# Kernel tuning notes

Hardware: AMD Instinct MI355X
Metric: run time of the kernel (lower is better)

The kernel has to match this reference:

```python
import jax, jax.numpy as jnp
import numpy as np
from jax.scipy.special import logsumexp

D = 1024      # d_model
H = 8         # num_heads
N = 16        # state_dim
ITERS = 5     # sinkhorn_iters
TAU = 1.0
B, S = 4, 1024
EPS = 1e-5


def setup_inputs() -> dict:
    key = jax.random.key(0)
    ks = jax.random.split(key, 8)
    x = jax.random.normal(ks[0], (B, S, D), dtype=jnp.float32)
    ln_w = jnp.ones((D,), jnp.float32)
    ln_b = jnp.zeros((D,), jnp.float32)
    # perm_proj: normal std=0.01, zero bias
    Wp = 0.01 * jax.random.normal(ks[1], (D, H * N * N), dtype=jnp.float32)
    bp = jnp.zeros((H * N * N,), jnp.float32)
    # gate_proj: normal std=0.01, bias=2.0
    Wg = 0.01 * jax.random.normal(ks[2], (D, H * N), dtype=jnp.float32)
    bg = jnp.full((H * N,), 2.0, jnp.float32)
    # input_proj / output_proj: xavier uniform, zero bias
    lim_i = float(np.sqrt(6.0 / (D + H * N)))
    Wi = jax.random.uniform(ks[3], (D, H * N), jnp.float32, -lim_i, lim_i)
    bi = jnp.zeros((H * N,), jnp.float32)
    Wo = jax.random.uniform(ks[4], (H * N, D), jnp.float32, -lim_i, lim_i)
    bo = jnp.zeros((D,), jnp.float32)
    return {"x": x, "ln_w": ln_w, "ln_b": ln_b, "Wp": Wp, "bp": bp,
            "Wg": Wg, "bg": bg, "Wi": Wi, "bi": bi, "Wo": Wo, "bo": bo}


def _sinkhorn(log_alpha):
    # log-space Sinkhorn: alternate row/column normalization
    for _ in range(ITERS):
        log_alpha = log_alpha - logsumexp(log_alpha, axis=-1, keepdims=True)
        log_alpha = log_alpha - logsumexp(log_alpha, axis=-2, keepdims=True)
    return jnp.exp(log_alpha)


def reference(x, ln_w, ln_b, Wp, bp, Wg, bg, Wi, bi, Wo, bo):
    residual = x
    # LayerNorm
    mu = jnp.mean(x, axis=-1, keepdims=True)
    var = jnp.var(x, axis=-1, keepdims=True)
    xn = (x - mu) * jax.lax.rsqrt(var + EPS) * ln_w + ln_b
    # projections
    logits = ((xn @ Wp + bp).reshape(B, S, H, N, N)) / TAU
    gamma = jax.nn.sigmoid((xn @ Wg + bg).reshape(B, S, H, N))
    b_in = (xn @ Wi + bi).reshape(B, S, H, N)
    # Sinkhorn for all timesteps at once (independent of recurrent state)
    soft = _sinkhorn(logits)                      # [B,S,H,N,N]
    # sequential state update over time
    Ps = jnp.moveaxis(soft, 1, 0)                 # [S,B,H,N,N]
    gs = jnp.moveaxis(gamma, 1, 0)                # [S,B,H,N]
    bs = jnp.moveaxis(b_in, 1, 0)                 # [S,B,H,N]

    def step(h, inp):
        P, g, b = inp
        h_perm = jnp.einsum('bhij,bhj->bhi', P, h)
        h_new = g * h_perm + (1.0 - g) * b
        return h_new, h_new

    h0 = jnp.zeros((B, H, N), x.dtype)
    _, hs = jax.lax.scan(step, h0, (Ps, gs, bs))  # hs: [S,B,H,N]
    out = jnp.moveaxis(hs, 0, 1).reshape(B, S, H * N)
    out = out @ Wo + bo                           # dropout = identity (eval)
    return residual + out
```

## Files before the change

kernel.cpp:

```cpp
#include <hip/hip_runtime.h>
#include <hip/hip_bf16.h>

#define D_    1024
#define H_    8
#define N_    16
#define B_    4
#define S_    1024
#define TOK   (B_*S_)
#define NPROJ 2304
#define CHUNK 32
#define NCHUNK (S_/CHUNK)
#define NCHAIN (B_*H_)

typedef __attribute__((ext_vector_type(8))) short bf16x8;
typedef __attribute__((ext_vector_type(4))) float f32x4;

typedef __attribute__((address_space(3))) void       as3_void;
typedef const __attribute__((address_space(1))) void as1_void;

__device__ __forceinline__ void gload_lds16(const void* g, void* l) {
    __builtin_amdgcn_global_load_lds((as1_void*)g, (as3_void*)l, 16, 0, 0);
}

__device__ __forceinline__ short f2bf(float f) {
    unsigned u = __builtin_bit_cast(unsigned, f);
    unsigned r = 0x7FFFu + ((u >> 16) & 1u);
    return (short)((u + r) >> 16);
}
__device__ __forceinline__ float bf2f(short s) {
    unsigned u = ((unsigned)(unsigned short)s) << 16;
    return __builtin_bit_cast(float, u);
}

template <int IMM>
__device__ __forceinline__ float swzf(float x) {
    return __builtin_bit_cast(float,
        __builtin_amdgcn_ds_swizzle(__builtin_bit_cast(int, x), IMM));
}
__device__ __forceinline__ float bpermf(int addr, float x) {
    return __builtin_bit_cast(float,
        __builtin_amdgcn_ds_bpermute(addr, __builtin_bit_cast(int, x)));
}
template <int CTRL>
__device__ __forceinline__ float dppmov(float x) {
    return __builtin_bit_cast(float,
        __builtin_amdgcn_update_dpp(0, __builtin_bit_cast(int, x),
                                    CTRL, 0xF, 0xF, true));
}
#define DPP_QX1  0xB1
#define DPP_QX2  0x4E
#define DPP_HMIR 0x141
#define DPP_ROR8 0x128

__global__ __launch_bounds__(256) void tcast_all(const float* __restrict__ Wp,
                                                 const float* __restrict__ Wg,
                                                 const float* __restrict__ Wi,
                                                 const float* __restrict__ Wo,
                                                 short* __restrict__ WcatT,
                                                 short* __restrict__ WoT) {
    int id = blockIdx.x;
    const float* src; short* dst; int srcW, Ksz, n_off, bx, by;
    if (id < 2048)      { src = Wp; dst = WcatT; srcW = 2048; Ksz = 1024; n_off = 0;
                          bx = id & 63;  by = id >> 6; }
    else if (id < 2176) { int q = id - 2048; src = Wg; dst = WcatT; srcW = 128; Ksz = 1024;
                          n_off = 2048; bx = q & 3; by = q >> 2; }
    else if (id < 2304) { int q = id - 2176; src = Wi; dst = WcatT; srcW = 128; Ksz = 1024;
                          n_off = 2176; bx = q & 3; by = q >> 2; }
    else                { int q = id - 2304; src = Wo; dst = WoT; srcW = 1024; Ksz = 128;
                          n_off = 0; bx = q & 31; by = q >> 5; }
    __shared__ float tile[32][33];
    int n0 = bx * 32, k0 = by * 32;
    int r  = threadIdx.x >> 3;
    int c4 = (threadIdx.x & 7) * 4;
    float4 v = *(const float4*)(src + (size_t)(k0 + r) * srcW + n0 + c4);
    tile[r][c4+0] = v.x; tile[r][c4+1] = v.y; tile[r][c4+2] = v.z; tile[r][c4+3] = v.w;
    __syncthreads();
    short4 o;
    o.x = f2bf(tile[c4+0][r]); o.y = f2bf(tile[c4+1][r]);
    o.z = f2bf(tile[c4+2][r]); o.w = f2bf(tile[c4+3][r]);
    *(short4*)(dst + (size_t)(n_off + n0 + r) * Ksz + k0 + c4) = o;
}

__global__ __launch_bounds__(256) void ln_kernel(const float* __restrict__ x,
                                                 const float* __restrict__ w,
                                                 const float* __restrict__ b,
                                                 short* __restrict__ xn) {
    int row = blockIdx.x;
    int t = threadIdx.x;
    const float* xr = x + (size_t)row * D_;
    float4 v = *(const float4*)(xr + t * 4);
    float s  = v.x + v.y + v.z + v.w;
    float s2 = v.x*v.x + v.y*v.y + v.z*v.z + v.w*v.w;
    #pragma unroll
    for (int m = 1; m < 64; m <<= 1) { s += __shfl_xor(s, m); s2 += __shfl_xor(s2, m); }
    __shared__ float ps[4], ps2[4];
    if ((t & 63) == 0) { ps[t >> 6] = s; ps2[t >> 6] = s2; }
    __syncthreads();
    s  = ps[0] + ps[1] + ps[2] + ps[3];
    s2 = ps2[0] + ps2[1] + ps2[2] + ps2[3];
    float mu  = s * (1.0f / D_);
    float var = s2 * (1.0f / D_) - mu * mu;
    float inv = rsqrtf(var + 1e-5f);
    float4 wv = *(const float4*)(w + t * 4);
    float4 bv = *(const float4*)(b + t * 4);
    short4 o;
    o.x = f2bf((v.x - mu) * inv * wv.x + bv.x);
    o.y = f2bf((v.y - mu) * inv * wv.y + bv.y);
    o.z = f2bf((v.z - mu) * inv * wv.z + bv.z);
    o.w = f2bf((v.w - mu) * inv * wv.w + bv.w);
    *(short4*)(xn + (size_t)row * D_ + t * 4) = o;
}

template <int MODE>
__global__ __launch_bounds__(512) void gemm_bt(const short* __restrict__ A,
                                               const short* __restrict__ BT,
                                               void* __restrict__ Cout,
                                               int M, int N, int K,
                                               const float* __restrict__ bias0,
                                               const float* __restrict__ bias1,
                                               const float* __restrict__ bias2,
                                               const float* __restrict__ resid) {
    __shared__ short lA[2][128 * 32];
    __shared__ short lB[2][128 * 32];
    const int nwg = gridDim.x;
    const int cpx = nwg >> 3;
    const int orig = blockIdx.x;
    const int wg = (orig & 7) * cpx + (orig >> 3);
    const int ntn = N >> 7;
    const int m0 = (wg / ntn) * 128, n0 = (wg % ntn) * 128;
    const int t = threadIdx.x, w = t >> 6, l = t & 63;
    const int wm = w >> 2, wn = w & 3;
    const int sr = l >> 2;
    const int sg = (l & 3) ^ ((l >> 3) & 3);
    const int fr = l & 15, fg = l >> 4;
    const int frag_off = fr * 32 + 8 * (fg ^ ((fr >> 1) & 3));

    f32x4 acc[4][2];
    #pragma unroll
    for (int mi = 0; mi < 4; ++mi)
        #pragma unroll
        for (int ni = 0; ni < 2; ++ni) acc[mi][ni] = (f32x4){0.f, 0.f, 0.f, 0.f};

    auto STAGE = [&](int bi, int k0) {
        int row = w * 16 + sr;
        gload_lds16(A  + (size_t)(m0 + row) * K + k0 + sg * 8, &lA[bi][w * 512]);
        gload_lds16(BT + (size_t)(n0 + row) * K + k0 + sg * 8, &lB[bi][w * 512]);
    };

    const int NT = K >> 5;
    STAGE(0, 0);
    if (NT > 1) STAGE(1, 32);
    asm volatile("s_waitcnt vmcnt(2)" ::: "memory");
    __builtin_amdgcn_s_barrier();

    int cur = 0;
    for (int kt = 0; kt < NT; ++kt) {
        bf16x8 af[4], bfr[2];
        #pragma unroll
        for (int mi = 0; mi < 4; ++mi)
            af[mi] = *(const bf16x8*)(&lA[cur][(wm * 4 + mi) * 512] + frag_off);
        #pragma unroll
        for (int ni = 0; ni < 2; ++ni)
            bfr[ni] = *(const bf16x8*)(&lB[cur][(wn * 2 + ni) * 512] + frag_off);
        asm volatile("s_waitcnt lgkmcnt(0)" ::: "memory");
        __builtin_amdgcn_sched_barrier(0);
        __builtin_amdgcn_s_barrier();
        if (kt + 2 < NT) STAGE(cur, (kt + 2) << 5);
        __builtin_amdgcn_s_setprio(1);
        #pragma unroll
        for (int mi = 0; mi < 4; ++mi)
            #pragma unroll
            for (int ni = 0; ni < 2; ++ni)
                acc[mi][ni] = __builtin_amdgcn_mfma_f32_16x16x32_bf16(af[mi], bfr[ni], acc[mi][ni], 0, 0, 0);
        __builtin_amdgcn_s_setprio(0);
        if (kt + 1 < NT) {
            if (kt + 2 < NT) asm volatile("s_waitcnt vmcnt(2)" ::: "memory");
            else             asm volatile("s_waitcnt vmcnt(0)" ::: "memory");
            __builtin_amdgcn_sched_barrier(0);
            __builtin_amdgcn_s_barrier();
        }
        cur ^= 1;
    }

    const int cr = (l >> 4) * 4, cc = l & 15;
    #pragma unroll
    for (int mi = 0; mi < 4; ++mi)
        #pragma unroll
        for (int ni = 0; ni < 2; ++ni) {
            int col = n0 + wn * 32 + ni * 16 + cc;
            float badd;
            if (MODE == 0)
                badd = (col < 2048) ? bias0[col] : (col < 2176 ? bias1[col - 2048] : bias2[col - 2176]);
            else
                badd = bias0[col];
            #pragma unroll
            for (int e = 0; e < 4; ++e) {
                int row = m0 + wm * 64 + mi * 16 + cr + e;
                float vout = acc[mi][ni][e] + badd;
                if (MODE == 0) {
                    ((short*)Cout)[(size_t)row * N + col] = f2bf(vout);
                } else {
                    vout += resid[(size_t)row * N + col];
                    ((float*)Cout)[(size_t)row * N + col] = vout;
                }
            }
        }
}

__global__ __launch_bounds__(256) void sinkhorn_kernel(const short* __restrict__ Cp,
                                                       short* __restrict__ Ahat,
                                                       float* __restrict__ u) {
    int w = threadIdx.x >> 6, l = threadIdx.x & 63;
    int id = blockIdx.x * 4 + w;
    int r = id >> 3, hh = id & 7;
    int a = l >> 3, b = l & 7;
    const short* base = Cp + (size_t)r * NPROJ + hh * 256;
    short2 q0 = *(const short2*)(base + (2 * a)     * 16 + 2 * b);
    short2 q1 = *(const short2*)(base + (2 * a + 1) * 16 + 2 * b);
    float p00 = __expf(bf2f(q0.x)), p01 = __expf(bf2f(q0.y));
    float p10 = __expf(bf2f(q1.x)), p11 = __expf(bf2f(q1.y));
    const int a32 = ((l ^ 32) << 2);
    #pragma unroll
    for (int it = 0; it < 5; ++it) {
        float r0 = p00 + p01, r1 = p10 + p11;
        r0 += dppmov<DPP_QX1>(r0);  r1 += dppmov<DPP_QX1>(r1);
        r0 += dppmov<DPP_QX2>(r0);  r1 += dppmov<DPP_QX2>(r1);
        r0 += dppmov<DPP_HMIR>(r0); r1 += dppmov<DPP_HMIR>(r1);
        float i0 = __builtin_amdgcn_rcpf(r0), i1 = __builtin_amdgcn_rcpf(r1);
        p00 *= i0; p01 *= i0; p10 *= i1; p11 *= i1;
        float c0 = p00 + p10, c1 = p01 + p11;
        c0 += dppmov<DPP_ROR8>(c0); c1 += dppmov<DPP_ROR8>(c1);
        c0 += swzf<0x401F>(c0);     c1 += swzf<0x401F>(c1);
        c0 += bpermf(a32, c0);      c1 += bpermf(a32, c1);
        float j0 = __builtin_amdgcn_rcpf(c0), j1 = __builtin_amdgcn_rcpf(c1);
        p00 *= j0; p10 *= j0; p01 *= j1; p11 *= j1;
    }
    short2 gp = *(const short2*)(Cp + (size_t)r * NPROJ + 2048 + hh * 16 + 2 * a);
    short2 bn = *(const short2*)(Cp + (size_t)r * NPROJ + 2176 + hh * 16 + 2 * a);
    float g0 = 1.f / (1.f + __expf(-bf2f(gp.x)));
    float g1 = 1.f / (1.f + __expf(-bf2f(gp.y)));
    short2 o0, o1;
    o0.x = f2bf(g0 * p00); o0.y = f2bf(g0 * p01);
    o1.x = f2bf(g1 * p10); o1.y = f2bf(g1 * p11);
    short* Ao = Ahat + (size_t)id * 256;
    *(short2*)(Ao + (2 * a)     * 16 + 2 * b) = o0;
    *(short2*)(Ao + (2 * a + 1) * 16 + 2 * b) = o1;
    if (b == 0) {
        float2 uo;
        uo.x = (1.f - g0) * bf2f(bn.x);
        uo.y = (1.f - g1) * bf2f(bn.y);
        *(float2*)(u + (size_t)id * 16 + 2 * a) = uo;
    }
}

__global__ __launch_bounds__(64) void pass1_kernel(const short* __restrict__ Ahat,
                                                   const float* __restrict__ u,
                                                   float* __restrict__ Mc,
                                                   float* __restrict__ vc) {
    __shared__ short lAh[CHUNK * 256];
    __shared__ float lu[CHUNK * 16];
    int unit = blockIdx.x;
    int chain = unit >> 5, c = unit & 31;
    int b = chain >> 3, hh = chain & 7;
    int l = threadIdx.x;
    int j = l & 15, g = l >> 4;
    const size_t id0 = ((size_t)(b * S_ + c * CHUNK)) * H_ + hh;

    #pragma unroll
    for (int q = 0; q < 16; ++q) {
        int m = q * 2 + (l >> 5);
        gload_lds16(Ahat + (id0 + (size_t)m * H_) * 256 + (l & 31) * 8,
                    (char*)lAh + q * 1024);
    }
    #pragma unroll
    for (int q = 0; q < 2; ++q) {
        int sl = q * 16 + (l >> 2);
        gload_lds16(u + (id0 + (size_t)sl * H_) * 16 + (l & 3) * 4,
                    (char*)lu + q * 1024);
    }
    asm volatile("s_waitcnt vmcnt(0)" ::: "memory");

    bf16x8 mb = {0,0,0,0,0,0,0,0};
    bf16x8 vb = {0,0,0,0,0,0,0,0};
    #pragma unroll
    for (int e = 0; e < 4; ++e) if (4 * g + e == j) mb[e] = (short)0x3F80;
    const f32x4 zero = {0.f, 0.f, 0.f, 0.f};
    f32x4 d = zero, dv = zero;
    #pragma unroll 4
    for (int tt = 0; tt < CHUNK; ++tt) {
        short4 pa = *(const short4*)(&lAh[tt * 256 + j * 16 + g * 4]);
        bf16x8 af = {0,0,0,0,0,0,0,0};
        af[0] = pa.x; af[1] = pa.y; af[2] = pa.z; af[3] = pa.w;
        d  = __builtin_amdgcn_mfma_f32_16x16x32_bf16(af, mb, zero, 0, 0, 0);
        dv = __builtin_amdgcn_mfma_f32_16x16x32_bf16(af, vb, zero, 0, 0, 0);
        if (j == 0) {
            dv[0] += lu[tt * 16 + 4 * g + 0];
            dv[1] += lu[tt * 16 + 4 * g + 1];
            dv[2] += lu[tt * 16 + 4 * g + 2];
            dv[3] += lu[tt * 16 + 4 * g + 3];
        }
        mb[0] = f2bf(d[0]);  mb[1] = f2bf(d[1]);  mb[2] = f2bf(d[2]);  mb[3] = f2bf(d[3]);
        vb[0] = f2bf(dv[0]); vb[1] = f2bf(dv[1]); vb[2] = f2bf(dv[2]); vb[3] = f2bf(dv[3]);
    }
    float* Mo = Mc + (size_t)unit * 256;
    #pragma unroll
    for (int e = 0; e < 4; ++e) Mo[(4 * g + e) * 16 + j] = d[e];
    if (j == 0) {
        #pragma unroll
        for (int e = 0; e < 4; ++e) vc[(size_t)unit * 16 + 4 * g + e] = dv[e];
    }
}

__global__ __launch_bounds__(64) void pass2_kernel(const float* __restrict__ Mc,
                                                   const float* __restrict__ vc,
                                                   float* __restrict__ hstart) {
    int chain = blockIdx.x;
    int l = threadIdx.x, i = l & 15;
    float h = 0.f;
    size_t u0 = (size_t)chain * NCHUNK;
    const float* Mr = Mc + u0 * 256 + i * 16;
    float4 m0 = *(const float4*)(Mr);
    float4 m1 = *(const float4*)(Mr + 4);
    float4 m2 = *(const float4*)(Mr + 8);
    float4 m3 = *(const float4*)(Mr + 12);
    float vcur = vc[u0 * 16 + i];
    for (int c = 0; c < NCHUNK; ++c) {
        size_t unit = u0 + c;
        if (l < 16) hstart[unit * 16 + i] = h;
        float4 n0 = m0, n1 = m1, n2 = m2, n3 = m3;
        float vnext = vcur;
        if (c + 1 < NCHUNK) {
            const float* Mn = Mc + (unit + 1) * 256 + i * 16;
            n0 = *(const float4*)(Mn);
            n1 = *(const float4*)(Mn + 4);
            n2 = *(const float4*)(Mn + 8);
            n3 = *(const float4*)(Mn + 12);
            vnext = vc[(unit + 1) * 16 + i];
        }
        float acc = vcur;
        acc += m0.x * __shfl(h, 0)  + m0.y * __shfl(h, 1)  + m0.z * __shfl(h, 2)  + m0.w * __shfl(h, 3);
        acc += m1.x * __shfl(h, 4)  + m1.y * __shfl(h, 5)  + m1.z * __shfl(h, 6)  + m1.w * __shfl(h, 7);
        acc += m2.x * __shfl(h, 8)  + m2.y * __shfl(h, 9)  + m2.z * __shfl(h, 10) + m2.w * __shfl(h, 11);
        acc += m3.x * __shfl(h, 12) + m3.y * __shfl(h, 13) + m3.z * __shfl(h, 14) + m3.w * __shfl(h, 15);
        h = acc;
        m0 = n0; m1 = n1; m2 = n2; m3 = n3; vcur = vnext;
    }
}

__global__ __launch_bounds__(64) void pass3_kernel(const short* __restrict__ Ahat,
                                                   const float* __restrict__ u,
                                                   const float* __restrict__ hstart,
                                                   short* __restrict__ hs) {
    __shared__ short lAh[CHUNK * 256];
    __shared__ float lu[CHUNK * 16];
    int unit = blockIdx.x;
    int chain = unit >> 5, c = unit & 31;
    int b = chain >> 3, hh = chain & 7;
    int l = threadIdx.x, i = l & 15, g = l >> 4;
    const size_t id0 = ((size_t)(b * S_ + c * CHUNK)) * H_ + hh;

    #pragma unroll
    for (int q = 0; q < 16; ++q) {
        int m = q * 2 + (l >> 5);
        gload_lds16(Ahat + (id0 + (size_t)m * H_) * 256 + (l & 31) * 8,
                    (char*)lAh + q * 1024);
    }
    #pragma unroll
    for (int q = 0; q < 2; ++q) {
        int sl = q * 16 + (l >> 2);
        gload_lds16(u + (id0 + (size_t)sl * H_) * 16 + (l & 3) * 4,
                    (char*)lu + q * 1024);
    }
    float4 h0 = *(const float4*)(hstart + (size_t)unit * 16 + g * 4);
    float h_0 = h0.x, h_1 = h0.y, h_2 = h0.z, h_3 = h0.w;
    asm volatile("s_waitcnt vmcnt(0)" ::: "memory");

    #pragma unroll 4
    for (int tt = 0; tt < CHUNK; ++tt) {
        size_t r = (size_t)b * S_ + c * CHUNK + tt;
        short4 pa = *(const short4*)(&lAh[tt * 256 + i * 16 + g * 4]);
        float part = bf2f(pa.x) * h_0 + bf2f(pa.y) * h_1 + bf2f(pa.z) * h_2 + bf2f(pa.w) * h_3;
        part += __shfl_xor(part, 16);
        part += __shfl_xor(part, 32);
        float hnew = part + lu[tt * 16 + i];
        if (g == 0) hs[r * 128 + hh * 16 + i] = f2bf(hnew);
        h_0 = __shfl(hnew, 4 * g + 0);
        h_1 = __shfl(hnew, 4 * g + 1);
        h_2 = __shfl(hnew, 4 * g + 2);
        h_3 = __shfl(hnew, 4 * g + 3);
    }
}

extern "C" void kernel_launch(void* const* d_in, const int* in_sizes, int n_in,
                              void* d_out, int out_size, void* d_ws, size_t ws_size,
                              hipStream_t stream) {
    const float* x    = (const float*)d_in[0];
    const float* ln_w = (const float*)d_in[1];
    const float* ln_b = (const float*)d_in[2];
    const float* Wp   = (const float*)d_in[3];
    const float* bp   = (const float*)d_in[4];
    const float* Wg   = (const float*)d_in[5];
    const float* bg   = (const float*)d_in[6];
    const float* Wi   = (const float*)d_in[7];
    const float* bi   = (const float*)d_in[8];
    const float* Wo   = (const float*)d_in[9];
    const float* bo   = (const float*)d_in[10];
    float* out = (float*)d_out;

    char* ws = (char*)d_ws;
    constexpr size_t OFF_WCATT = 0;
    constexpr size_t OFF_WOT   = OFF_WCATT + (size_t)NPROJ * D_ * 2;
    constexpr size_t OFF_XN    = OFF_WOT   + (size_t)D_ * 128 * 2;
    constexpr size_t OFF_CP    = OFF_XN    + (size_t)TOK * D_ * 2;
    constexpr size_t OFF_AHAT  = OFF_CP    + (size_t)TOK * NPROJ * 2;
    constexpr size_t OFF_U     = OFF_AHAT  + (size_t)TOK * H_ * 256 * 2;
    constexpr size_t OFF_MC    = OFF_U     + (size_t)TOK * H_ * 16 * 4;
    constexpr size_t OFF_VC    = OFF_MC    + (size_t)NCHAIN * NCHUNK * 256 * 4;
    constexpr size_t OFF_HST   = OFF_VC    + (size_t)NCHAIN * NCHUNK * 16 * 4;
    constexpr size_t OFF_HS    = OFF_HST   + (size_t)NCHAIN * NCHUNK * 16 * 4;

    short* WcatT = (short*)(ws + OFF_WCATT);
    short* WoT   = (short*)(ws + OFF_WOT);
    short* xn    = (short*)(ws + OFF_XN);
    short* Cp    = (short*)(ws + OFF_CP);
    short* Ahat  = (short*)(ws + OFF_AHAT);
    float* u     = (float*)(ws + OFF_U);
    float* Mc    = (float*)(ws + OFF_MC);
    float* vc    = (float*)(ws + OFF_VC);
    float* hst   = (float*)(ws + OFF_HST);
    short* hs    = (short*)(ws + OFF_HS);

    tcast_all<<<2432, 256, 0, stream>>>(Wp, Wg, Wi, Wo, WcatT, WoT);
    ln_kernel<<<TOK, 256, 0, stream>>>(x, ln_w, ln_b, xn);
    gemm_bt<0><<<(NPROJ / 128) * (TOK / 128), 512, 0, stream>>>(
        xn, WcatT, (void*)Cp, TOK, NPROJ, 1024, bp, bg, bi, nullptr);
    sinkhorn_kernel<<<(TOK * H_) / 4, 256, 0, stream>>>(Cp, Ahat, u);
    pass1_kernel<<<NCHAIN * NCHUNK, 64, 0, stream>>>(Ahat, u, Mc, vc);
    pass2_kernel<<<NCHAIN, 64, 0, stream>>>(Mc, vc, hst);
    pass3_kernel<<<NCHAIN * NCHUNK, 64, 0, stream>>>(Ahat, u, hst, hs);
    gemm_bt<1><<<(D_ / 128) * (TOK / 128), 512, 0, stream>>>(
        hs, WoT, (void*)out, TOK, D_, 128, bo, nullptr, nullptr, x);
}
```

Measured before the change: 102.9 us.

## Fuse three scan passes into one cooperative kernel and merge prep kernels

```diff
diff --git a/kernel.cpp b/kernel.cpp
--- a/kernel.cpp
+++ b/kernel.cpp
@@ -1,5 +1,8 @@
 #include <hip/hip_runtime.h>
 #include <hip/hip_bf16.h>
+#include <hip/hip_cooperative_groups.h>
+
+namespace cg = cooperative_groups;
 
 #define D_    1024
 #define H_    8
@@ -52,63 +55,64 @@
 #define DPP_HMIR 0x141
 #define DPP_ROR8 0x128
 
-__global__ __launch_bounds__(256) void tcast_all(const float* __restrict__ Wp,
-                                                 const float* __restrict__ Wg,
-                                                 const float* __restrict__ Wi,
-                                                 const float* __restrict__ Wo,
-                                                 short* __restrict__ WcatT,
-                                                 short* __restrict__ WoT) {
+__global__ __launch_bounds__(256) void prep_kernel(const float* __restrict__ Wp,
+                                                   const float* __restrict__ Wg,
+                                                   const float* __restrict__ Wi,
+                                                   const float* __restrict__ Wo,
+                                                   short* __restrict__ WcatT,
+                                                   short* __restrict__ WoT,
+                                                   const float* __restrict__ x,
+                                                   const float* __restrict__ lnw,
+                                                   const float* __restrict__ lnb,
+                                                   short* __restrict__ xn) {
     int id = blockIdx.x;
-    const float* src; short* dst; int srcW, Ksz, n_off, bx, by;
-    if (id < 2048)      { src = Wp; dst = WcatT; srcW = 2048; Ksz = 1024; n_off = 0;
-                          bx = id & 63;  by = id >> 6; }
-    else if (id < 2176) { int q = id - 2048; src = Wg; dst = WcatT; srcW = 128; Ksz = 1024;
-                          n_off = 2048; bx = q & 3; by = q >> 2; }
-    else if (id < 2304) { int q = id - 2176; src = Wi; dst = WcatT; srcW = 128; Ksz = 1024;
-                          n_off = 2176; bx = q & 3; by = q >> 2; }
-    else                { int q = id - 2304; src = Wo; dst = WoT; srcW = 1024; Ksz = 128;
-                          n_off = 0; bx = q & 31; by = q >> 5; }
-    __shared__ float tile[32][33];
-    int n0 = bx * 32, k0 = by * 32;
-    int r  = threadIdx.x >> 3;
-    int c4 = (threadIdx.x & 7) * 4;
-    float4 v = *(const float4*)(src + (size_t)(k0 + r) * srcW + n0 + c4);
-    tile[r][c4+0] = v.x; tile[r][c4+1] = v.y; tile[r][c4+2] = v.z; tile[r][c4+3] = v.w;
-    __syncthreads();
-    short4 o;
-    o.x = f2bf(tile[c4+0][r]); o.y = f2bf(tile[c4+1][r]);
-    o.z = f2bf(tile[c4+2][r]); o.w = f2bf(tile[c4+3][r]);
-    *(short4*)(dst + (size_t)(n_off + n0 + r) * Ksz + k0 + c4) = o;
-}
-
-__global__ __launch_bounds__(256) void ln_kernel(const float* __restrict__ x,
-                                                 const float* __restrict__ w,
-                                                 const float* __restrict__ b,
-                                                 short* __restrict__ xn) {
-    int row = blockIdx.x;
-    int t = threadIdx.x;
-    const float* xr = x + (size_t)row * D_;
-    float4 v = *(const float4*)(xr + t * 4);
-    float s  = v.x + v.y + v.z + v.w;
-    float s2 = v.x*v.x + v.y*v.y + v.z*v.z + v.w*v.w;
-    #pragma unroll
-    for (int m = 1; m < 64; m <<= 1) { s += __shfl_xor(s, m); s2 += __shfl_xor(s2, m); }
-    __shared__ float ps[4], ps2[4];
-    if ((t & 63) == 0) { ps[t >> 6] = s; ps2[t >> 6] = s2; }
-    __syncthreads();
-    s  = ps[0] + ps[1] + ps[2] + ps[3];
-    s2 = ps2[0] + ps2[1] + ps2[2] + ps2[3];
-    float mu  = s * (1.0f / D_);
-    float var = s2 * (1.0f / D_) - mu * mu;
-    float inv = rsqrtf(var + 1e-5f);
-    float4 wv = *(const float4*)(w + t * 4);
-    float4 bv = *(const float4*)(b + t * 4);
-    short4 o;
-    o.x = f2bf((v.x - mu) * inv * wv.x + bv.x);
-    o.y = f2bf((v.y - mu) * inv * wv.y + bv.y);
-    o.z = f2bf((v.z - mu) * inv * wv.z + bv.z);
-    o.w = f2bf((v.w - mu) * inv * wv.w + bv.w);
-    *(short4*)(xn + (size_t)row * D_ + t * 4) = o;
+    if (id < 2432) {
+        const float* src; short* dst; int srcW, Ksz, n_off, bx, by;
+        if (id < 2048)      { src = Wp; dst = WcatT; srcW = 2048; Ksz = 1024; n_off = 0;
+                              bx = id & 63;  by = id >> 6; }
+        else if (id < 2176) { int q = id - 2048; src = Wg; dst = WcatT; srcW = 128; Ksz = 1024;
+                              n_off = 2048; bx = q & 3; by = q >> 2; }
+        else if (id < 2304) { int q = id - 2176; src = Wi; dst = WcatT; srcW = 128; Ksz = 1024;
+                              n_off = 2176; bx = q & 3; by = q >> 2; }
+        else                { int q = id - 2304; src = Wo; dst = WoT; srcW = 1024; Ksz = 128;
+                              n_off = 0; bx = q & 31; by = q >> 5; }
+        __shared__ float tile[32][33];
+        int n0 = bx * 32, k0 = by * 32;
+        int r  = threadIdx.x >> 3;
+        int c4 = (threadIdx.x & 7) * 4;
+        float4 v = *(const float4*)(src + (size_t)(k0 + r) * srcW + n0 + c4);
+        tile[r][c4+0] = v.x; tile[r][c4+1] = v.y; tile[r][c4+2] = v.z; tile[r][c4+3] = v.w;
+        __syncthreads();
+        short4 o;
+        o.x = f2bf(tile[c4+0][r]); o.y = f2bf(tile[c4+1][r]);
+        o.z = f2bf(tile[c4+2][r]); o.w = f2bf(tile[c4+3][r]);
+        *(short4*)(dst + (size_t)(n_off + n0 + r) * Ksz + k0 + c4) = o;
+    } else {
+        int row = id - 2432;
+        int t = threadIdx.x;
+        const float* xr = x + (size_t)row * D_;
+        float4 v = *(const float4*)(xr + t * 4);
+        float s  = v.x + v.y + v.z + v.w;
+        float s2 = v.x*v.x + v.y*v.y + v.z*v.z + v.w*v.w;
+        #pragma unroll
+        for (int m = 1; m < 64; m <<= 1) { s += __shfl_xor(s, m); s2 += __shfl_xor(s2, m); }
+        __shared__ float ps[4], ps2[4];
+        if ((t & 63) == 0) { ps[t >> 6] = s; ps2[t >> 6] = s2; }
+        __syncthreads();
+        s  = ps[0] + ps[1] + ps[2] + ps[3];
+        s2 = ps2[0] + ps2[1] + ps2[2] + ps2[3];
+        float mu  = s * (1.0f / D_);
+        float var = s2 * (1.0f / D_) - mu * mu;
+        float inv = rsqrtf(var + 1e-5f);
+        float4 wv = *(const float4*)(lnw + t * 4);
+        float4 bv = *(const float4*)(lnb + t * 4);
+        short4 o;
+        o.x = f2bf((v.x - mu) * inv * wv.x + bv.x);
+        o.y = f2bf((v.y - mu) * inv * wv.y + bv.y);
+        o.z = f2bf((v.z - mu) * inv * wv.z + bv.z);
+        o.w = f2bf((v.w - mu) * inv * wv.w + bv.w);
+        *(short4*)(xn + (size_t)row * D_ + t * 4) = o;
+    }
 }
 
 template <int MODE>
@@ -253,17 +257,19 @@
     }
 }
 
-__global__ __launch_bounds__(64) void pass1_kernel(const short* __restrict__ Ahat,
-                                                   const float* __restrict__ u,
-                                                   float* __restrict__ Mc,
-                                                   float* __restrict__ vc) {
+__global__ __launch_bounds__(64) void scan_coop(const short* __restrict__ Ahat,
+                                                const float* __restrict__ u,
+                                                float* __restrict__ Mc,
+                                                float* __restrict__ vc,
+                                                float* __restrict__ hstart,
+                                                short* __restrict__ hs) {
     __shared__ short lAh[CHUNK * 256];
     __shared__ float lu[CHUNK * 16];
-    int unit = blockIdx.x;
-    int chain = unit >> 5, c = unit & 31;
-    int b = chain >> 3, hh = chain & 7;
-    int l = threadIdx.x;
-    int j = l & 15, g = l >> 4;
+    const int unit = blockIdx.x;
+    const int chain = unit >> 5, c = unit & 31;
+    const int b = chain >> 3, hh = chain & 7;
+    const int l = threadIdx.x;
+    const int j = l & 15, g = l >> 4;
     const size_t id0 = ((size_t)(b * S_ + c * CHUNK)) * H_ + hh;
 
     #pragma unroll
@@ -280,114 +286,93 @@
     }
     asm volatile("s_waitcnt vmcnt(0)" ::: "memory");
 
-    bf16x8 mb = {0,0,0,0,0,0,0,0};
-    bf16x8 vb = {0,0,0,0,0,0,0,0};
-    #pragma unroll
-    for (int e = 0; e < 4; ++e) if (4 * g + e == j) mb[e] = (short)0x3F80;
-    const f32x4 zero = {0.f, 0.f, 0.f, 0.f};
-    f32x4 d = zero, dv = zero;
-    #pragma unroll 4
-    for (int tt = 0; tt < CHUNK; ++tt) {
-        short4 pa = *(const short4*)(&lAh[tt * 256 + j * 16 + g * 4]);
-        bf16x8 af = {0,0,0,0,0,0,0,0};
-        af[0] = pa.x; af[1] = pa.y; af[2] = pa.z; af[3] = pa.w;
-        d  = __builtin_amdgcn_mfma_f32_16x16x32_bf16(af, mb, zero, 0, 0, 0);
-        dv = __builtin_amdgcn_mfma_f32_16x16x32_bf16(af, vb, zero, 0, 0, 0);
+    {
+        bf16x8 mb = {0,0,0,0,0,0,0,0};
+        bf16x8 vb = {0,0,0,0,0,0,0,0};
+        #pragma unroll
+        for (int e = 0; e < 4; ++e) if (4 * g + e == j) mb[e] = (short)0x3F80;
+        const f32x4 zero = {0.f, 0.f, 0.f, 0.f};
+        f32x4 d = zero, dv = zero;
+        #pragma unroll 4
+        for (int tt = 0; tt < CHUNK; ++tt) {
+            short4 pa = *(const short4*)(&lAh[tt * 256 + j * 16 + g * 4]);
+            bf16x8 af = {0,0,0,0,0,0,0,0};
+            af[0] = pa.x; af[1] = pa.y; af[2] = pa.z; af[3] = pa.w;
+            d  = __builtin_amdgcn_mfma_f32_16x16x32_bf16(af, mb, zero, 0, 0, 0);
+            dv = __builtin_amdgcn_mfma_f32_16x16x32_bf16(af, vb, zero, 0, 0, 0);
+            if (j == 0) {
+                dv[0] += lu[tt * 16 + 4 * g + 0];
+                dv[1] += lu[tt * 16 + 4 * g + 1];
+                dv[2] += lu[tt * 16 + 4 * g + 2];
+                dv[3] += lu[tt * 16 + 4 * g + 3];
+            }
+            mb[0] = f2bf(d[0]);  mb[1] = f2bf(d[1]);  mb[2] = f2bf(d[2]);  mb[3] = f2bf(d[3]);
+            vb[0] = f2bf(dv[0]); vb[1] = f2bf(dv[1]); vb[2] = f2bf(dv[2]); vb[3] = f2bf(dv[3]);
+        }
+        float* Mo = Mc + (size_t)unit * 256;
+        #pragma unroll
+        for (int e = 0; e < 4; ++e) Mo[(4 * g + e) * 16 + j] = d[e];
         if (j == 0) {
-            dv[0] += lu[tt * 16 + 4 * g + 0];
-            dv[1] += lu[tt * 16 + 4 * g + 1];
-            dv[2] += lu[tt * 16 + 4 * g + 2];
-            dv[3] += lu[tt * 16 + 4 * g + 3];
-        }
-        mb[0] = f2bf(d[0]);  mb[1] = f2bf(d[1]);  mb[2] = f2bf(d[2]);  mb[3] = f2bf(d[3]);
-        vb[0] = f2bf(dv[0]); vb[1] = f2bf(dv[1]); vb[2] = f2bf(dv[2]); vb[3] = f2bf(dv[3]);
-    }
-    float* Mo = Mc + (size_t)unit * 256;
-    #pragma unroll
-    for (int e = 0; e < 4; ++e) Mo[(4 * g + e) * 16 + j] = d[e];
-    if (j == 0) {
-        #pragma unroll
-        for (int e = 0; e < 4; ++e) vc[(size_t)unit * 16 + 4 * g + e] = dv[e];
-    }
-}
-
-__global__ __launch_bounds__(64) void pass2_kernel(const float* __restrict__ Mc,
-                                                   const float* __restrict__ vc,
-                                                   float* __restrict__ hstart) {
-    int chain = blockIdx.x;
-    int l = threadIdx.x, i = l & 15;
-    float h = 0.f;
-    size_t u0 = (size_t)chain * NCHUNK;
-    const float* Mr = Mc + u0 * 256 + i * 16;
-    float4 m0 = *(const float4*)(Mr);
-    float4 m1 = *(const float4*)(Mr + 4);
-    float4 m2 = *(const float4*)(Mr + 8);
-    float4 m3 = *(const float4*)(Mr + 12);
-    float vcur = vc[u0 * 16 + i];
-    for (int c = 0; c < NCHUNK; ++c) {
-        size_t unit = u0 + c;
-        if (l < 16) hstart[unit * 16 + i] = h;
-        float4 n0 = m0, n1 = m1, n2 = m2, n3 = m3;
-        float vnext = vcur;
-        if (c + 1 < NCHUNK) {
-            const float* Mn = Mc + (unit + 1) * 256 + i * 16;
-            n0 = *(const float4*)(Mn);
-            n1 = *(const float4*)(Mn + 4);
-            n2 = *(const float4*)(Mn + 8);
-            n3 = *(const float4*)(Mn + 12);
-            vnext = vc[(unit + 1) * 16 + i];
-        }
-        float acc = vcur;
-        acc += m0.x * __shfl(h, 0)  + m0.y * __shfl(h, 1)  + m0.z * __shfl(h, 2)  + m0.w * __shfl(h, 3);
-        acc += m1.x * __shfl(h, 4)  + m1.y * __shfl(h, 5)  + m1.z * __shfl(h, 6)  + m1.w * __shfl(h, 7);
-        acc += m2.x * __shfl(h, 8)  + m2.y * __shfl(h, 9)  + m2.z * __shfl(h, 10) + m2.w * __shfl(h, 11);
-        acc += m3.x * __shfl(h, 12) + m3.y * __shfl(h, 13) + m3.z * __shfl(h, 14) + m3.w * __shfl(h, 15);
-        h = acc;
-        m0 = n0; m1 = n1; m2 = n2; m3 = n3; vcur = vnext;
-    }
-}
-
-__global__ __launch_bounds__(64) void pass3_kernel(const short* __restrict__ Ahat,
-                                                   const float* __restrict__ u,
-                                                   const float* __restrict__ hstart,
-                                                   short* __restrict__ hs) {
-    __shared__ short lAh[CHUNK * 256];
-    __shared__ float lu[CHUNK * 16];
-    int unit = blockIdx.x;
-    int chain = unit >> 5, c = unit & 31;
-    int b = chain >> 3, hh = chain & 7;
-    int l = threadIdx.x, i = l & 15, g = l >> 4;
-    const size_t id0 = ((size_t)(b * S_ + c * CHUNK)) * H_ + hh;
-
-    #pragma unroll
-    for (int q = 0; q < 16; ++q) {
-        int m = q * 2 + (l >> 5);
-        gload_lds16(Ahat + (id0 + (size_t)m * H_) * 256 + (l & 31) * 8,
-                    (char*)lAh + q * 1024);
-    }
-    #pragma unroll
-    for (int q = 0; q < 2; ++q) {
-        int sl = q * 16 + (l >> 2);
-        gload_lds16(u + (id0 + (size_t)sl * H_) * 16 + (l & 3) * 4,
-                    (char*)lu + q * 1024);
-    }
-    float4 h0 = *(const float4*)(hstart + (size_t)unit * 16 + g * 4);
-    float h_0 = h0.x, h_1 = h0.y, h_2 = h0.z, h_3 = h0.w;
-    asm volatile("s_waitcnt vmcnt(0)" ::: "memory");
-
-    #pragma unroll 4
-    for (int tt = 0; tt < CHUNK; ++tt) {
-        size_t r = (size_t)b * S_ + c * CHUNK + tt;
-        short4 pa = *(const short4*)(&lAh[tt * 256 + i * 16 + g * 4]);
-        float part = bf2f(pa.x) * h_0 + bf2f(pa.y) * h_1 + bf2f(pa.z) * h_2 + bf2f(pa.w) * h_3;
-        part += __shfl_xor(part, 16);
-        part += __shfl_xor(part, 32);
-        float hnew = part + lu[tt * 16 + i];
-        if (g == 0) hs[r * 128 + hh * 16 + i] = f2bf(hnew);
-        h_0 = __shfl(hnew, 4 * g + 0);
-        h_1 = __shfl(hnew, 4 * g + 1);
-        h_2 = __shfl(hnew, 4 * g + 2);
-        h_3 = __shfl(hnew, 4 * g + 3);
+            #pragma unroll
+            for (int e = 0; e < 4; ++e) vc[(size_t)unit * 16 + 4 * g + e] = dv[e];
+        }
+    }
+    __threadfence();
+    cg::this_grid().sync();
+
+    if (c == 0) {
+        const int i = j;
+        float h = 0.f;
+        size_t u0 = (size_t)chain * NCHUNK;
+        const float* Mr = Mc + u0 * 256 + i * 16;
+        float4 m0 = *(const float4*)(Mr);
+        float4 m1 = *(const float4*)(Mr + 4);
+        float4 m2 = *(const float4*)(Mr + 8);
+        float4 m3 = *(const float4*)(Mr + 12);
+        float vcur = vc[u0 * 16 + i];
+        for (int cc2 = 0; cc2 < NCHUNK; ++cc2) {
+            size_t un = u0 + cc2;
+            if (l < 16) hstart[un * 16 + i] = h;
+            float4 n0 = m0, n1 = m1, n2 = m2, n3 = m3;
+            float vnext = vcur;
+            if (cc2 + 1 < NCHUNK) {
+                const float* Mn = Mc + (un + 1) * 256 + i * 16;
+                n0 = *(const float4*)(Mn);
+                n1 = *(const float4*)(Mn + 4);
+                n2 = *(const float4*)(Mn + 8);
+                n3 = *(const float4*)(Mn + 12);
+                vnext = vc[(un + 1) * 16 + i];
+            }
+            float acc = vcur;
+            acc += m0.x * __shfl(h, 0)  + m0.y * __shfl(h, 1)  + m0.z * __shfl(h, 2)  + m0.w * __shfl(h, 3);
+            acc += m1.x * __shfl(h, 4)  + m1.y * __shfl(h, 5)  + m1.z * __shfl(h, 6)  + m1.w * __shfl(h, 7);
+            acc += m2.x * __shfl(h, 8)  + m2.y * __shfl(h, 9)  + m2.z * __shfl(h, 10) + m2.w * __shfl(h, 11);
+            acc += m3.x * __shfl(h, 12) + m3.y * __shfl(h, 13) + m3.z * __shfl(h, 14) + m3.w * __shfl(h, 15);
+            h = acc;
+            m0 = n0; m1 = n1; m2 = n2; m3 = n3; vcur = vnext;
+        }
+    }
+    __threadfence();
+    cg::this_grid().sync();
+
+    {
+        const int i = j;
+        float4 h0 = *(const float4*)(hstart + (size_t)unit * 16 + g * 4);
+        float h_0 = h0.x, h_1 = h0.y, h_2 = h0.z, h_3 = h0.w;
+        #pragma unroll 4
+        for (int tt = 0; tt < CHUNK; ++tt) {
+            size_t r = (size_t)b * S_ + c * CHUNK + tt;
+            short4 pa = *(const short4*)(&lAh[tt * 256 + i * 16 + g * 4]);
+            float part = bf2f(pa.x) * h_0 + bf2f(pa.y) * h_1 + bf2f(pa.z) * h_2 + bf2f(pa.w) * h_3;
+            part += __shfl_xor(part, 16);
+            part += __shfl_xor(part, 32);
+            float hnew = part + lu[tt * 16 + i];
+            if (g == 0) hs[r * 128 + hh * 16 + i] = f2bf(hnew);
+            h_0 = __shfl(hnew, 4 * g + 0);
+            h_1 = __shfl(hnew, 4 * g + 1);
+            h_2 = __shfl(hnew, 4 * g + 2);
+            h_3 = __shfl(hnew, 4 * g + 3);
+        }
     }
 }
 
@@ -430,14 +415,19 @@
     float* hst   = (float*)(ws + OFF_HST);
     short* hs    = (short*)(ws + OFF_HS);
 
-    tcast_all<<<2432, 256, 0, stream>>>(Wp, Wg, Wi, Wo, WcatT, WoT);
-    ln_kernel<<<TOK, 256, 0, stream>>>(x, ln_w, ln_b, xn);
+    prep_kernel<<<2432 + TOK, 256, 0, stream>>>(Wp, Wg, Wi, Wo, WcatT, WoT,
+                                                x, ln_w, ln_b, xn);
     gemm_bt<0><<<(NPROJ / 128) * (TOK / 128), 512, 0, stream>>>(
         xn, WcatT, (void*)Cp, TOK, NPROJ, 1024, bp, bg, bi, nullptr);
     sinkhorn_kernel<<<(TOK * H_) / 4, 256, 0, stream>>>(Cp, Ahat, u);
-    pass1_kernel<<<NCHAIN * NCHUNK, 64, 0, stream>>>(Ahat, u, Mc, vc);
-    pass2_kernel<<<NCHAIN, 64, 0, stream>>>(Mc, vc, hst);
-    pass3_kernel<<<NCHAIN * NCHUNK, 64, 0, stream>>>(Ahat, u, hst, hs);
+    {
+        const short* a0 = Ahat; const float* a1 = u;
+        float* a2 = Mc; float* a3 = vc; float* a4 = hst; short* a5 = hs;
+        void* kargs[6] = {&a0, &a1, &a2, &a3, &a4, &a5};
+        hipLaunchCooperativeKernel((const void*)scan_coop,
+                                   dim3(NCHAIN * NCHUNK), dim3(64),
+                                   kargs, 0, stream);
+    }
     gemm_bt<1><<<(D_ / 128) * (TOK / 128), 512, 0, stream>>>(
         hs, WoT, (void*)out, TOK, D_, 128, bo, nullptr, nullptr, x);
 }
```

Result: slower. 382.5 us (+271.7%).
